# Performance work log

Measured on AMD Instinct MI355X. Metric: run time of the kernel, lower is better.

The kernel has to match this reference:

```python
import jax, jax.numpy as jnp
import numpy as np

H = 768  # bert-base hidden size; match MLP width = 2*H = 1536


def setup_inputs() -> dict:
    key = jax.random.key(0)
    ks = jax.random.split(key, 6)
    B, S = 2, 256
    std = 0.02  # TruncatedNormal(stddev=initializer_range)
    return {
        "hidden": jax.random.normal(ks[0], (B, S, H), dtype=jnp.float32),
        "w_start": jax.random.normal(ks[1], (H, 1), dtype=jnp.float32) * std,
        "b_start": jnp.zeros((1,), jnp.float32),
        "w_end": jax.random.normal(ks[2], (H, 1), dtype=jnp.float32) * std,
        "b_end": jnp.zeros((1,), jnp.float32),
        "w1": jax.random.normal(ks[3], (2 * H, 2 * H), dtype=jnp.float32) * std,
        "b1": jnp.zeros((2 * H,), jnp.float32),
        "w2": jax.random.normal(ks[4], (2 * H, 1), dtype=jnp.float32) * std,
        "b2": jnp.zeros((1,), jnp.float32),
    }


def reference(hidden, w_start, b_start, w_end, b_end, w1, b1, w2, b2):
    # hidden: [B, S, H] = BERT sequence output (dropout disabled at inference)
    start_logits = hidden @ w_start + b_start  # [B, S, 1]
    end_logits = hidden @ w_end + b_end        # [B, S, 1]

    # Pairwise span features: concat(row_i, col_j) along last dim, fed to dense1.
    # concat([row, col]) @ w1 == row @ w1[:H] + col @ w1[H:], so we split w1 and
    # broadcast-add instead of materializing the [B,S,S,2H] concat tile.
    row_proj = hidden @ w1[:H]   # [B, S, 2H] (start-token contribution)
    col_proj = hidden @ w1[H:]   # [B, S, 2H] (end-token contribution)
    pre = row_proj[:, :, None, :] + col_proj[:, None, :, :] + b1  # [B, S, S, 2H]
    act = jax.nn.gelu(pre, approximate=False)  # keras 'gelu' is exact
    match_logits = act @ w2 + b2  # [B, S, S, 1]
    return start_logits, end_logits, match_logits
```

## Files before the change

### kernel.cpp

```cpp
#include <hip/hip_runtime.h>
#include <stdint.h>

typedef __attribute__((ext_vector_type(8))) __bf16 bf16x8;
typedef __attribute__((ext_vector_type(4))) float  floatx4;
typedef __attribute__((ext_vector_type(4))) unsigned int uint4v;
typedef __attribute__((ext_vector_type(2))) unsigned int uint2v;
typedef __attribute__((ext_vector_type(4))) float  float4v;
typedef __attribute__((ext_vector_type(2))) _Float16 half2v;
typedef unsigned int u32;

__device__ __forceinline__ unsigned short f2bf(float f) {
  union { float f; unsigned int u; } x; x.f = f;
  unsigned int r = x.u + 0x7fffu + ((x.u >> 16) & 1u);
  return (unsigned short)(r >> 16);
}

__global__ __launch_bounds__(256) void proj_kernel(
    const float* __restrict__ hidden, const float* __restrict__ w1,
    const float* __restrict__ b1, unsigned short* __restrict__ wsR,
    unsigned short* __restrict__ wsC,
    const float* __restrict__ w_start, const float* __restrict__ b_start,
    const float* __restrict__ w_end, const float* __restrict__ b_end,
    const float* __restrict__ b2, float* __restrict__ out) {
  const int tid  = threadIdx.x;
  if (blockIdx.y == 16) {
    if (blockIdx.x >= 32) {
      float v = b2[0];
      float4v vv = {v, v, v, v};
      int base = (blockIdx.x - 32) * 8192 + tid * 4;
#pragma unroll
      for (int itr = 0; itr < 8; ++itr)
        *(float4v*)(out + 1024 + base + itr * 1024) = vv;
      return;
    }
    const int lane = tid & 63;
    const int wv   = tid >> 6;
    const int wg   = blockIdx.x * 4 + wv;
    float wsv[12], wev[12];
#pragma unroll
    for (int t = 0; t < 12; ++t) {
      wsv[t] = w_start[lane + 64 * t];
      wev[t] = w_end[lane + 64 * t];
    }
    const float bs = b_start[0];
    const float be = b_end[0];
#pragma unroll
    for (int r = 0; r < 4; ++r) {
      int row = wg * 4 + r;
      const float* h = hidden + (size_t)row * 768;
      float ps = 0.f, pe = 0.f;
#pragma unroll
      for (int t = 0; t < 12; ++t) {
        float hv = h[lane + 64 * t];
        ps += hv * wsv[t];
        pe += hv * wev[t];
      }
#pragma unroll
      for (int off = 32; off >= 1; off >>= 1) {
        ps += __shfl_xor(ps, off, 64);
        pe += __shfl_xor(pe, off, 64);
      }
      if (lane == 0) { out[row] = ps + bs; out[512 + row] = pe + be; }
    }
    return;
  }

  __shared__ short As[4 * 32 * 8];
  __shared__ short Bs[4 * 64 * 8];

  const int lane = tid & 63;
  const int wave = tid >> 6;
  const int wr = wave >> 1, wc = wave & 1;
  const int m0 = blockIdx.y * 32;
  const int n0g = blockIdx.x * 64;
  const bool isR = (n0g < 1536);
  const int kbase = isR ? 0 : 768;
  const int n0 = isR ? n0g : (n0g - 1536);
  const int q = lane >> 4, l15 = lane & 15;

  floatx4 acc0 = {}, acc1 = {};

  const int a_row = tid >> 3;
  const int a_s   = tid & 7;
  const int b_n   = tid & 63;
  const int b_kg  = tid >> 6;

  const float* hrow = hidden + (size_t)(m0 + a_row) * 768 + a_s * 4;
  const float* bcol = w1 + (size_t)(kbase + b_kg * 8) * 1536 + n0 + b_n;

  float4v hv = *(const float4v*)(hrow);
  float bv[8];
#pragma unroll
  for (int a = 0; a < 8; ++a) bv[a] = bcol[(size_t)a * 1536];

  const int aq = a_s >> 1;
  const int aj = (a_s & 1) * 4;

  for (int ko = 0; ko < 768; ko += 32) {
    uint2v au;
    au[0] = (u32)f2bf(hv[0]) | ((u32)f2bf(hv[1]) << 16);
    au[1] = (u32)f2bf(hv[2]) | ((u32)f2bf(hv[3]) << 16);
    *(uint2v*)(&As[(aq * 32 + a_row) * 8 + aj]) = au;
    uint4v pv;
#pragma unroll
    for (int a = 0; a < 4; ++a) {
      u32 lo = f2bf(bv[2 * a]);
      u32 hi = f2bf(bv[2 * a + 1]);
      pv[a] = lo | (hi << 16);
    }
    *(uint4v*)(&Bs[(b_kg * 64 + b_n) * 8]) = pv;
    __syncthreads();

    if (ko + 32 < 768) {
      hv = *(const float4v*)(hrow + ko + 32);
      const float* bp = bcol + (size_t)(ko + 32) * 1536;
#pragma unroll
      for (int a = 0; a < 8; ++a) bv[a] = bp[(size_t)a * 1536];
    }

    bf16x8 af  = *(const bf16x8*)(&As[(q * 32 + 16 * wr + l15) * 8]);
    bf16x8 bg0 = *(const bf16x8*)(&Bs[(q * 64 + 32 * wc + l15) * 8]);
    bf16x8 bg1 = *(const bf16x8*)(&Bs[(q * 64 + 32 * wc + 16 + l15) * 8]);
    acc0 = __builtin_amdgcn_mfma_f32_16x16x32_bf16(af, bg0, acc0, 0, 0, 0);
    acc1 = __builtin_amdgcn_mfma_f32_16x16x32_bf16(af, bg1, acc1, 0, 0, 0);
    __syncthreads();
  }

  unsigned short* outp = isR ? wsR : wsC;
#pragma unroll
  for (int ni = 0; ni < 2; ++ni) {
    const floatx4& ac = ni ? acc1 : acc0;
    int col = n0 + 32 * wc + 16 * ni + l15;
    float bias = isR ? b1[col] : 0.0f;
#pragma unroll
    for (int r = 0; r < 4; ++r) {
      int rowg = m0 + 16 * wr + q * 4 + r;
      outp[(size_t)rowg * 1536 + col] = f2bf(ac[r] + bias);
    }
  }
}

__device__ __forceinline__ u32 ph_add(u32 a, u32 b) {
  u32 d; asm("v_pk_add_f16 %0, %1, %2" : "=v"(d) : "v"(a), "v"(b)); return d;
}
__device__ __forceinline__ u32 ph_mul(u32 a, u32 b) {
  u32 d; asm("v_pk_mul_f16 %0, %1, %2" : "=v"(d) : "v"(a), "v"(b)); return d;
}
__device__ __forceinline__ u32 ph_fma(u32 a, u32 b, u32 c) {
  u32 d; asm("v_pk_fma_f16 %0, %1, %2, %3" : "=v"(d) : "v"(a), "v"(b), "v"(c)); return d;
}
__device__ __forceinline__ u32 ph_max(u32 a, u32 b) {
  u32 d; asm("v_pk_max_f16 %0, %1, %2" : "=v"(d) : "v"(a), "v"(b)); return d;
}
__device__ __forceinline__ u32 ph_min(u32 a, u32 b) {
  u32 d; asm("v_pk_min_f16 %0, %1, %2" : "=v"(d) : "v"(a), "v"(b)); return d;
}
__device__ __forceinline__ u32 h2c(float f) {
  _Float16 h = (_Float16)f;
  unsigned short s = __builtin_bit_cast(unsigned short, h);
  return (u32)s | ((u32)s << 16);
}

__device__ __forceinline__ void gelu_pair(float& acc, u32 r, u32 c, u32 w,
                                          u32 C0c, u32 C1c, u32 C2c, u32 C3c,
                                          u32 LOc, u32 HIc, u32 Hc) {
  u32 x  = ph_add(r, c);
  u32 xc = ph_min(ph_max(x, LOc), HIc);
  u32 u  = ph_mul(xc, xc);
  u32 p  = ph_fma(u, ph_fma(u, ph_fma(u, C3c, C2c), C1c), C0c);
  u32 t  = ph_fma(xc, p, Hc);
  u32 g  = ph_mul(x, t);
  acc = __builtin_amdgcn_fdot2(__builtin_bit_cast(half2v, g),
                               __builtin_bit_cast(half2v, w), acc, false);
}

__device__ __forceinline__ uint4v bf8_to_h8(uint4v v) {
  uint4v o;
#pragma unroll
  for (int a = 0; a < 4; ++a) {
    union { unsigned int u; float f; } lo, hi;
    lo.u = v[a] << 16;
    hi.u = v[a] & 0xffff0000u;
    auto h = __builtin_amdgcn_cvt_pkrtz(lo.f, hi.f);
    o[a] = __builtin_bit_cast(unsigned int, h);
  }
  return o;
}

__global__ __launch_bounds__(512) void match_kernel(
    const unsigned short* __restrict__ wsR,
    const unsigned short* __restrict__ wsC,
    const float* __restrict__ w2,
    float* __restrict__ outm) {
  __shared__ u32 RsU[2][32 * 68];
  __shared__ u32 CsU[2][64 * 68];
  __shared__ u32 WsU[2][64];

  const int tid = threadIdx.x;
  const int jt = blockIdx.x;
  const int it = blockIdx.y;
  const int bz = blockIdx.z >> 2;
  const int kb4 = blockIdx.z & 3;
  const int Kb0 = kb4 * 384;

  const int rg  = tid >> 5;
  const int cg  = tid & 31;
  const int srow = tid >> 4;
  const int sseg = tid & 15;

  const u32 C0c = h2c(0.39103831f);
  const u32 C1c = h2c(-0.05415410f);
  const u32 C2c = h2c(0.00461682f);
  const u32 C3c = h2c(-1.51033e-4f);
  const u32 LOc = h2c(-3.5f);
  const u32 HIc = h2c(3.5f);
  const u32 Hc  = h2c(0.5f);

  float a0 = 0.f, a1 = 0.f, b0 = 0.f, b1 = 0.f;

  const unsigned short* gR  = wsR + (size_t)(bz * 256 + it * 32 + srow) * 1536 + sseg * 8;
  const unsigned short* gC0 = wsC + (size_t)(bz * 256 + jt * 64 + srow) * 1536 + sseg * 8;
  const unsigned short* gC1 = gC0 + (size_t)32 * 1536;

  auto wr = [&](int buf, uint4v pR, uint4v pC0, uint4v pC1, float w0, float w1) {
    *(uint4v*)(&RsU[buf][srow * 68 + sseg * 4]) = bf8_to_h8(pR);
    *(uint4v*)(&CsU[buf][srow * 68 + sseg * 4]) = bf8_to_h8(pC0);
    *(uint4v*)(&CsU[buf][(srow + 32) * 68 + sseg * 4]) = bf8_to_h8(pC1);
    if (tid < 64) {
      auto h = __builtin_amdgcn_cvt_pkrtz(w0, w1);
      WsU[buf][tid] = __builtin_bit_cast(u32, h);
    }
  };
  auto comp = [&](int buf) {
    const u32* rap = &RsU[buf][(2 * rg) * 68];
    const u32* rbp = rap + 68;
    const u32* c0p = &CsU[buf][cg * 68];
    const u32* c1p = c0p + 32 * 68;
    const u32* wp  = &WsU[buf][0];
#pragma unroll 4
    for (int ks = 0; ks < 16; ++ks) {
      uint4v ra = *(const uint4v*)(rap + ks * 4);
      uint4v rb = *(const uint4v*)(rbp + ks * 4);
      uint4v wv = *(const uint4v*)(wp + ks * 4);
      uint4v cv = *(const uint4v*)(c0p + ks * 4);
#pragma unroll
      for (int p = 0; p < 4; ++p) {
        gelu_pair(a0, ra[p], cv[p], wv[p], C0c, C1c, C2c, C3c, LOc, HIc, Hc);
        gelu_pair(b0, rb[p], cv[p], wv[p], C0c, C1c, C2c, C3c, LOc, HIc, Hc);
      }
      uint4v cw = *(const uint4v*)(c1p + ks * 4);
#pragma unroll
      for (int p = 0; p < 4; ++p) {
        gelu_pair(a1, ra[p], cw[p], wv[p], C0c, C1c, C2c, C3c, LOc, HIc, Hc);
        gelu_pair(b1, rb[p], cw[p], wv[p], C0c, C1c, C2c, C3c, LOc, HIc, Hc);
      }
    }
  };

  uint4v pR  = *(const uint4v*)(gR + Kb0);
  uint4v pC0 = *(const uint4v*)(gC0 + Kb0);
  uint4v pC1 = *(const uint4v*)(gC1 + Kb0);
  float pw0 = 0.f, pw1 = 0.f;
  if (tid < 64) { pw0 = w2[Kb0 + 2 * tid]; pw1 = w2[Kb0 + 2 * tid + 1]; }
  wr(0, pR, pC0, pC1, pw0, pw1);
  __syncthreads();

  pR  = *(const uint4v*)(gR + Kb0 + 128);
  pC0 = *(const uint4v*)(gC0 + Kb0 + 128);
  pC1 = *(const uint4v*)(gC1 + Kb0 + 128);
  if (tid < 64) { pw0 = w2[Kb0 + 128 + 2 * tid]; pw1 = w2[Kb0 + 128 + 2 * tid + 1]; }
  comp(0);
  wr(1, pR, pC0, pC1, pw0, pw1);
  __syncthreads();

  pR  = *(const uint4v*)(gR + Kb0 + 256);
  pC0 = *(const uint4v*)(gC0 + Kb0 + 256);
  pC1 = *(const uint4v*)(gC1 + Kb0 + 256);
  if (tid < 64) { pw0 = w2[Kb0 + 256 + 2 * tid]; pw1 = w2[Kb0 + 256 + 2 * tid + 1]; }
  comp(1);
  wr(0, pR, pC0, pC1, pw0, pw1);
  __syncthreads();

  comp(0);

  const size_t rowA = (size_t)(bz * 256 + it * 32 + 2 * rg);
  const size_t base = rowA * 256 + jt * 64 + cg;
  unsafeAtomicAdd(&outm[base +  0], a0);
  unsafeAtomicAdd(&outm[base + 32], a1);
  unsafeAtomicAdd(&outm[base + 256 +  0], b0);
  unsafeAtomicAdd(&outm[base + 256 + 32], b1);
}

extern "C" void kernel_launch(void* const* d_in, const int* in_sizes, int n_in,
                              void* d_out, int out_size, void* d_ws, size_t ws_size,
                              hipStream_t stream) {
  const float* hidden  = (const float*)d_in[0];
  const float* w_start = (const float*)d_in[1];
  const float* b_start = (const float*)d_in[2];
  const float* w_end   = (const float*)d_in[3];
  const float* b_end   = (const float*)d_in[4];
  const float* w1      = (const float*)d_in[5];
  const float* b1      = (const float*)d_in[6];
  const float* w2      = (const float*)d_in[7];
  const float* b2      = (const float*)d_in[8];

  float* out = (float*)d_out;
  char* ws = (char*)d_ws;
  unsigned short* wsR = (unsigned short*)(ws);
  unsigned short* wsC = (unsigned short*)(ws + 1572864);

  proj_kernel<<<dim3(48, 17), dim3(256), 0, stream>>>(
      hidden, w1, b1, wsR, wsC, w_start, b_start, w_end, b_end, b2, out);
  match_kernel<<<dim3(4, 8, 8), dim3(512), 0, stream>>>(wsR, wsC, w2, out + 1024);
}
```

Measured before the change: 126.2 us.

## Pre-convert w1 to bf16 tiles and double-buffer projection GEMM with global_load_lds

Adds a separate kernel that converts w1 once per call into a bf16, k-grouped layout in workspace. The projection GEMM then streams B tiles straight into LDS with global_load_lds and uses double-buffered 64-wide K steps, where it previously did per-block fp32 loads and conversions at 32-wide K steps. The aim is to cut redundant conversion work, reduce syncs, and overlap loads with MFMA. The cost is an extra kernel launch and an extra pass over w1 through memory.

```diff
diff --git a/kernel.cpp b/kernel.cpp
--- a/kernel.cpp
+++ b/kernel.cpp
@@ -15,8 +15,29 @@
   return (unsigned short)(r >> 16);
 }
 
+__device__ __forceinline__ void gll16(const unsigned short* g, unsigned short* l) {
+  __builtin_amdgcn_global_load_lds(
+      (const __attribute__((address_space(1))) unsigned int*)g,
+      (__attribute__((address_space(3))) unsigned int*)l, 16, 0, 0);
+}
+
+__global__ __launch_bounds__(256) void convert_kernel(
+    const float* __restrict__ w1, unsigned short* __restrict__ Wfmt) {
+  const int n  = blockIdx.x * 256 + threadIdx.x;
+  const int qg = blockIdx.y;
+  const float* src = w1 + (size_t)(qg * 8) * 1536 + n;
+  uint4v o;
+#pragma unroll
+  for (int a = 0; a < 4; ++a) {
+    u32 lo = f2bf(src[(size_t)(2 * a) * 1536]);
+    u32 hi = f2bf(src[(size_t)(2 * a + 1) * 1536]);
+    o[a] = lo | (hi << 16);
+  }
+  *(uint4v*)(Wfmt + ((size_t)qg * 1536 + n) * 8) = o;
+}
+
 __global__ __launch_bounds__(256) void proj_kernel(
-    const float* __restrict__ hidden, const float* __restrict__ w1,
+    const float* __restrict__ hidden, const unsigned short* __restrict__ Wfmt,
     const float* __restrict__ b1, unsigned short* __restrict__ wsR,
     unsigned short* __restrict__ wsC,
     const float* __restrict__ w_start, const float* __restrict__ b_start,
@@ -65,8 +86,8 @@
     return;
   }
 
-  __shared__ short As[4 * 32 * 8];
-  __shared__ short Bs[4 * 64 * 8];
+  __shared__ unsigned short As2[2][8 * 32 * 8];
+  __shared__ unsigned short Bs2[2][8 * 64 * 8];
 
   const int lane = tid & 63;
   const int wave = tid >> 6;
@@ -74,57 +95,83 @@
   const int m0 = blockIdx.y * 32;
   const int n0g = blockIdx.x * 64;
   const bool isR = (n0g < 1536);
-  const int kbase = isR ? 0 : 768;
+  const int qgb = isR ? 0 : 96;
   const int n0 = isR ? n0g : (n0g - 1536);
-  const int q = lane >> 4, l15 = lane & 15;
+  const int q4 = lane >> 4, l15 = lane & 15;
 
   floatx4 acc0 = {}, acc1 = {};
 
   const int a_row = tid >> 3;
   const int a_s   = tid & 7;
-  const int b_n   = tid & 63;
-  const int b_kg  = tid >> 6;
-
+  const int aqh   = a_s >> 1;
+  const int aj    = (a_s & 1) * 4;
   const float* hrow = hidden + (size_t)(m0 + a_row) * 768 + a_s * 4;
-  const float* bcol = w1 + (size_t)(kbase + b_kg * 8) * 1536 + n0 + b_n;
-
-  float4v hv = *(const float4v*)(hrow);
-  float bv[8];
-#pragma unroll
-  for (int a = 0; a < 8; ++a) bv[a] = bcol[(size_t)a * 1536];
-
-  const int aq = a_s >> 1;
-  const int aj = (a_s & 1) * 4;
-
-  for (int ko = 0; ko < 768; ko += 32) {
-    uint2v au;
-    au[0] = (u32)f2bf(hv[0]) | ((u32)f2bf(hv[1]) << 16);
-    au[1] = (u32)f2bf(hv[2]) | ((u32)f2bf(hv[3]) << 16);
-    *(uint2v*)(&As[(aq * 32 + a_row) * 8 + aj]) = au;
-    uint4v pv;
-#pragma unroll
-    for (int a = 0; a < 4; ++a) {
-      u32 lo = f2bf(bv[2 * a]);
-      u32 hi = f2bf(bv[2 * a + 1]);
-      pv[a] = lo | (hi << 16);
-    }
-    *(uint4v*)(&Bs[(b_kg * 64 + b_n) * 8]) = pv;
+
+  const unsigned short* gB0 = Wfmt + ((size_t)(qgb + 2 * wave) * 1536 + n0 + lane) * 8;
+  const unsigned short* gB1 = Wfmt + ((size_t)(qgb + 2 * wave + 1) * 1536 + n0 + lane) * 8;
+  const size_t bstep = (size_t)8 * 1536 * 8;
+  unsigned short* lB0 = &Bs2[0][(2 * wave) * 512];
+  unsigned short* lB1 = &Bs2[0][(2 * wave + 1) * 512];
+  unsigned short* lB0b = &Bs2[1][(2 * wave) * 512];
+  unsigned short* lB1b = &Bs2[1][(2 * wave + 1) * 512];
+
+#define PACKA(BUF, H, V)                                                     \
+  {                                                                          \
+    uint2v au_;                                                              \
+    au_[0] = (u32)f2bf((V)[0]) | ((u32)f2bf((V)[1]) << 16);                  \
+    au_[1] = (u32)f2bf((V)[2]) | ((u32)f2bf((V)[3]) << 16);                  \
+    *(uint2v*)(&As2[BUF][(((H) * 4 + aqh) * 32 + a_row) * 8 + aj]) = au_;    \
+  }
+
+#define COMPUTE(BUF)                                                         \
+  {                                                                          \
+    _Pragma("unroll")                                                        \
+    for (int ko2 = 0; ko2 < 2; ++ko2) {                                      \
+      int qf = ko2 * 4 + q4;                                                 \
+      bf16x8 af  = *(const bf16x8*)(&As2[BUF][(qf * 32 + 16 * wr + l15) * 8]); \
+      bf16x8 bg0 = *(const bf16x8*)(&Bs2[BUF][(qf * 64 + 32 * wc + l15) * 8]); \
+      bf16x8 bg1 = *(const bf16x8*)(&Bs2[BUF][(qf * 64 + 32 * wc + 16 + l15) * 8]); \
+      acc0 = __builtin_amdgcn_mfma_f32_16x16x32_bf16(af, bg0, acc0, 0, 0, 0); \
+      acc1 = __builtin_amdgcn_mfma_f32_16x16x32_bf16(af, bg1, acc1, 0, 0, 0); \
+    }                                                                        \
+  }
+
+  gll16(gB0, lB0);
+  gll16(gB1, lB1);
+  float4v sA0 = *(const float4v*)(hrow);
+  float4v sA1 = *(const float4v*)(hrow + 32);
+  PACKA(0, 0, sA0); PACKA(0, 1, sA1);
+  float4v sB0 = *(const float4v*)(hrow + 64);
+  float4v sB1 = *(const float4v*)(hrow + 96);
+  __syncthreads();
+
+#pragma unroll
+  for (int kb = 0; kb < 12; kb += 2) {
+    if (kb + 1 < 12) {
+      gll16(gB0 + (size_t)(kb + 1) * bstep, lB0b);
+      gll16(gB1 + (size_t)(kb + 1) * bstep, lB1b);
+      PACKA(1, 0, sB0); PACKA(1, 1, sB1);
+    }
+    if (kb + 2 < 12) {
+      sA0 = *(const float4v*)(hrow + (kb + 2) * 64);
+      sA1 = *(const float4v*)(hrow + (kb + 2) * 64 + 32);
+    }
+    COMPUTE(0);
     __syncthreads();
-
-    if (ko + 32 < 768) {
-      hv = *(const float4v*)(hrow + ko + 32);
-      const float* bp = bcol + (size_t)(ko + 32) * 1536;
-#pragma unroll
-      for (int a = 0; a < 8; ++a) bv[a] = bp[(size_t)a * 1536];
-    }
-
-    bf16x8 af  = *(const bf16x8*)(&As[(q * 32 + 16 * wr + l15) * 8]);
-    bf16x8 bg0 = *(const bf16x8*)(&Bs[(q * 64 + 32 * wc + l15) * 8]);
-    bf16x8 bg1 = *(const bf16x8*)(&Bs[(q * 64 + 32 * wc + 16 + l15) * 8]);
-    acc0 = __builtin_amdgcn_mfma_f32_16x16x32_bf16(af, bg0, acc0, 0, 0, 0);
-    acc1 = __builtin_amdgcn_mfma_f32_16x16x32_bf16(af, bg1, acc1, 0, 0, 0);
+    if (kb + 2 < 12) {
+      gll16(gB0 + (size_t)(kb + 2) * bstep, lB0);
+      gll16(gB1 + (size_t)(kb + 2) * bstep, lB1);
+      PACKA(0, 0, sA0); PACKA(0, 1, sA1);
+    }
+    if (kb + 3 < 12) {
+      sB0 = *(const float4v*)(hrow + (kb + 3) * 64);
+      sB1 = *(const float4v*)(hrow + (kb + 3) * 64 + 32);
+    }
+    if (kb + 1 < 12) COMPUTE(1);
     __syncthreads();
   }
+#undef PACKA
+#undef COMPUTE
 
   unsigned short* outp = isR ? wsR : wsC;
 #pragma unroll
@@ -134,7 +181,7 @@
     float bias = isR ? b1[col] : 0.0f;
 #pragma unroll
     for (int r = 0; r < 4; ++r) {
-      int rowg = m0 + 16 * wr + q * 4 + r;
+      int rowg = m0 + 16 * wr + q4 * 4 + r;
       outp[(size_t)rowg * 1536 + col] = f2bf(ac[r] + bias);
     }
   }
@@ -306,10 +353,12 @@
 
   float* out = (float*)d_out;
   char* ws = (char*)d_ws;
-  unsigned short* wsR = (unsigned short*)(ws);
-  unsigned short* wsC = (unsigned short*)(ws + 1572864);
-
+  unsigned short* wsR  = (unsigned short*)(ws);
+  unsigned short* wsC  = (unsigned short*)(ws + 1572864);
+  unsigned short* Wfmt = (unsigned short*)(ws + 3145728);
+
+  convert_kernel<<<dim3(6, 192), dim3(256), 0, stream>>>(w1, Wfmt);
   proj_kernel<<<dim3(48, 17), dim3(256), 0, stream>>>(
-      hidden, w1, b1, wsR, wsC, w_start, b_start, w_end, b_end, b2, out);
+      hidden, Wfmt, b1, wsR, wsC, w_start, b_start, w_end, b_end, b2, out);
   match_kernel<<<dim3(4, 8, 8), dim3(512), 0, stream>>>(wsR, wsC, w2, out + 1024);
 }
```

Result: faster. 123.6 us (-2.1%).
